# Kernel optimization log

Hardware: AMD Instinct MI355X
Metric: run time of the kernel (lower is better)

The kernel has to match this reference:

```python
import jax, jax.numpy as jnp
import numpy as np
import math

D_MODEL = 1024
N_HEADS = 16
QKV_DIM = 1024
D_HEAD = QKV_DIM // N_HEADS


def setup_inputs() -> dict:
    key = jax.random.key(0)
    ks = jax.random.split(key, 10)
    B, S = 4, 2048
    lim = 1.0 / math.sqrt(D_MODEL)
    lim_o = 1.0 / math.sqrt(QKV_DIM)
    return {
        "x": jax.random.normal(ks[0], (B, S, D_MODEL), dtype=jnp.float32),
        "w_q": jax.random.uniform(ks[1], (QKV_DIM, D_MODEL), minval=-lim, maxval=lim, dtype=jnp.float32),
        "b_q": jax.random.uniform(ks[2], (QKV_DIM,), minval=-lim, maxval=lim, dtype=jnp.float32),
        "w_k": jax.random.uniform(ks[3], (QKV_DIM, D_MODEL), minval=-lim, maxval=lim, dtype=jnp.float32),
        "b_k": jax.random.uniform(ks[4], (QKV_DIM,), minval=-lim, maxval=lim, dtype=jnp.float32),
        "w_v": jax.random.uniform(ks[5], (QKV_DIM, D_MODEL), minval=-lim, maxval=lim, dtype=jnp.float32),
        "b_v": jax.random.uniform(ks[6], (QKV_DIM,), minval=-lim, maxval=lim, dtype=jnp.float32),
        "w_o": jax.random.uniform(ks[7], (D_MODEL, QKV_DIM), minval=-lim_o, maxval=lim_o, dtype=jnp.float32),
        "b_o": jax.random.uniform(ks[8], (D_MODEL,), minval=-lim_o, maxval=lim_o, dtype=jnp.float32),
        "temperature": jnp.ones((1,), dtype=jnp.float32),
        "q_scale": jnp.ones((N_HEADS,), dtype=jnp.float32),
    }


def reference(x, w_q, b_q, w_k, b_k, w_v, b_v, w_o, b_o, temperature, q_scale):
    B, S, _ = x.shape
    # QKV projections: [B,S,qkv_dim] -> [B,H,S,Dh]
    def proj(w, b):
        y = jnp.einsum('bsd,ed->bse', x, w) + b
        return y.reshape(B, S, N_HEADS, D_HEAD).transpose(0, 2, 1, 3)
    q = proj(w_q, b_q)
    k = proj(w_k, b_k)
    v = proj(w_v, b_v)
    scale = jnp.sqrt(jnp.float32(D_HEAD)) * temperature[0]
    scores = jnp.einsum('bhqd,bhkd->bhqk', q, k) / scale
    attn = jax.nn.softmax(scores, axis=-1)
    attn = attn * q_scale.reshape(1, N_HEADS, 1, 1)  # per-head post-softmax scale
    out = jnp.einsum('bhqk,bhkd->bhqd', attn, v)
    out = out.transpose(0, 2, 1, 3).reshape(B, S, QKV_DIM)
    return jnp.einsum('bse,de->bsd', out, w_o) + b_o
```

## Files before the change

kernel.cpp:

```cpp
#include <hip/hip_runtime.h>
#include <hip/hip_bf16.h>
#include <stdint.h>

typedef __bf16 bf16;
typedef __bf16 bf16x8 __attribute__((ext_vector_type(8)));
typedef __bf16 bf16x4 __attribute__((ext_vector_type(4)));
typedef float f32x4 __attribute__((ext_vector_type(4)));
typedef float f32x16 __attribute__((ext_vector_type(16)));

#define NB 4
#define SEQ 2048
#define DM 1024
#define NHEADS 16
#define DHEAD 64
#define MTOK (NB*SEQ)
#define NE 3072

__device__ __forceinline__ void gl_lds16(const bf16* g, bf16* l) {
  __builtin_amdgcn_global_load_lds(
      (const __attribute__((address_space(1))) void*)g,
      (__attribute__((address_space(3))) void*)l, 16, 0, 0);
}

__device__ __forceinline__ f32x16 zero16() {
  f32x16 z;
#pragma unroll
  for (int i=0;i<16;i++) z[i]=0.f;
  return z;
}

__global__ __launch_bounds__(256) void convert_kernel(
    const float* __restrict__ x,
    const float* __restrict__ wq, const float* __restrict__ wk,
    const float* __restrict__ wv, const float* __restrict__ wo,
    const float* __restrict__ bq, const float* __restrict__ bk,
    const float* __restrict__ bv,
    bf16* __restrict__ xb, bf16* __restrict__ wqkvb,
    bf16* __restrict__ wob, float* __restrict__ bqkv) {
  int tid = blockIdx.x*blockDim.x + threadIdx.x;
  int nt = gridDim.x*blockDim.x;
  const int NX4 = MTOK*DM/4;
  for (int i = tid; i < NX4; i += nt) {
    float4 v = ((const float4*)x)[i];
    ((bf16x4*)xb)[i] = bf16x4{(bf16)v.x,(bf16)v.y,(bf16)v.z,(bf16)v.w};
  }
  const int NW4 = DM*DM/4;
  for (int i = tid; i < NW4; i += nt) {
    float4 a = ((const float4*)wq)[i];
    ((bf16x4*)wqkvb)[i] = bf16x4{(bf16)a.x,(bf16)a.y,(bf16)a.z,(bf16)a.w};
    float4 b = ((const float4*)wk)[i];
    ((bf16x4*)wqkvb)[i+NW4] = bf16x4{(bf16)b.x,(bf16)b.y,(bf16)b.z,(bf16)b.w};
    float4 c = ((const float4*)wv)[i];
    ((bf16x4*)wqkvb)[i+2*NW4] = bf16x4{(bf16)c.x,(bf16)c.y,(bf16)c.z,(bf16)c.w};
    float4 d = ((const float4*)wo)[i];
    ((bf16x4*)wob)[i] = bf16x4{(bf16)d.x,(bf16)d.y,(bf16)d.z,(bf16)d.w};
  }
  for (int i = tid; i < DM; i += nt) {
    bqkv[i] = bq[i]; bqkv[i+DM] = bk[i]; bqkv[i+2*DM] = bv[i];
  }
}

template<int OUT_MODE>
__global__ __launch_bounds__(256) void gemm_deep(
    const bf16* __restrict__ A, const bf16* __restrict__ Bm,
    const float* __restrict__ bias, void* __restrict__ Cout,
    int M, int N, int K) {
  __shared__ bf16 As[2][128*64];
  __shared__ bf16 Bs[2][128*64];
  const int bm = blockIdx.x, bn = blockIdx.y;
  const int thr = threadIdx.x;
  const int w = thr>>6, lane = thr&63;
  const int wr = w>>1, wc = w&1;
  const int l4 = lane>>4, lm = lane&15;
  f32x4 acc[4][4];
#pragma unroll
  for (int m=0;m<4;m++)
#pragma unroll
    for (int n=0;n<4;n++) acc[m][n] = f32x4{0.f,0.f,0.f,0.f};

  const bf16* Abase = A + (size_t)bm*128*K;
  const bf16* Bbase = Bm + (size_t)bn*128*K;

  const int srow = thr>>3;
  const int sch  = ((thr&7) ^ (srow&7)) * 8;
  const bf16* Ag = Abase + (size_t)srow*K + sch;
  const bf16* Bg = Bbase + (size_t)srow*K + sch;
  const int dbase = thr*8;

  const int nk = K>>6;

  int aoff[2][4], boff[2][4];
#pragma unroll
  for (int ks=0;ks<2;ks++) {
#pragma unroll
    for (int m=0;m<4;m++) {
      const int r = wr*64 + m*16 + lm;
      aoff[ks][m] = r*64 + ((((ks<<2)|l4) ^ (lm&7))*8);
    }
#pragma unroll
    for (int n=0;n<4;n++) {
      const int r = wc*64 + n*16 + lm;
      boff[ks][n] = r*64 + ((((ks<<2)|l4) ^ (lm&7))*8);
    }
  }

#pragma unroll
  for (int c=0;c<4;c++) {
    gl_lds16(Ag + (size_t)c*32*K, &As[0][c*2048 + dbase]);
    gl_lds16(Bg + (size_t)c*32*K, &Bs[0][c*2048 + dbase]);
  }

  for (int kt=0; kt<nk; ++kt) {
    const int p = kt&1;
    const int st = (kt+1 < nk) ? kt+1 : 0;
    const size_t ko = (size_t)st*64;
#pragma unroll
    for (int c=0;c<4;c++) {
      gl_lds16(Ag + ko + (size_t)c*32*K, &As[p^1][c*2048 + dbase]);
      gl_lds16(Bg + ko + (size_t)c*32*K, &Bs[p^1][c*2048 + dbase]);
    }
    asm volatile("s_waitcnt vmcnt(8)" ::: "memory");
    __builtin_amdgcn_s_barrier();
    __builtin_amdgcn_sched_barrier(0);

    const bf16* Ac = As[p];
    const bf16* Bc = Bs[p];
    __builtin_amdgcn_s_setprio(1);
#pragma unroll
    for (int ks=0;ks<2;ks++) {
      bf16x8 af[4], bfr[4];
#pragma unroll
      for (int m=0;m<4;m++) af[m] = *(const bf16x8*)&Ac[aoff[ks][m]];
#pragma unroll
      for (int n=0;n<4;n++) bfr[n] = *(const bf16x8*)&Bc[boff[ks][n]];
#pragma unroll
      for (int m=0;m<4;m++)
#pragma unroll
        for (int n=0;n<4;n++)
          acc[m][n] = __builtin_amdgcn_mfma_f32_16x16x32_bf16(af[m], bfr[n], acc[m][n], 0, 0, 0);
    }
    __builtin_amdgcn_s_setprio(0);
    __builtin_amdgcn_s_barrier();
    __builtin_amdgcn_sched_barrier(0);
  }

  const int rbase = bm*128 + wr*64 + l4*4;
  const int cbase = bn*128 + wc*64;
#pragma unroll
  for (int n=0;n<4;n++) {
    const int col = cbase + n*16 + lm;
    const float bv = bias[col];
#pragma unroll
    for (int m=0;m<4;m++) {
#pragma unroll
      for (int j=0;j<4;j++) {
        const int row = rbase + m*16 + j;
        const float v = acc[m][n][j] + bv;
        if (OUT_MODE == 0) ((bf16*)Cout)[(size_t)row*N + col] = (bf16)v;
        else               ((float*)Cout)[(size_t)row*N + col] = v;
      }
    }
  }
}

__global__ __launch_bounds__(256) void transpose_v(const bf16* __restrict__ qkv,
                                                   bf16* __restrict__ vt) {
  __shared__ bf16 tile[64*72];
  const int s0 = blockIdx.x*64;
  const int bh = blockIdx.y;
  const bf16* src = qkv + (size_t)((bh>>4)*SEQ + s0)*NE + 2*DM + (bh&15)*64;
  const int thr = threadIdx.x;
#pragma unroll
  for (int i=0;i<2;i++) {
    int idx = thr + i*256;
    int row = idx>>3, part = idx&7;
    *(bf16x8*)&tile[row*72 + part*8] = *(const bf16x8*)(src + (size_t)row*NE + part*8);
  }
  __syncthreads();
  bf16* dst = vt + (size_t)bh*64*SEQ + s0;
#pragma unroll
  for (int i=0;i<2;i++) {
    int idx = thr + i*256;
    int d = idx>>3, part = idx&7;
    bf16x8 v;
#pragma unroll
    for (int j=0;j<8;j++) v[j] = tile[(part*8+j)*72 + d];
    *(bf16x8*)(dst + (size_t)d*SEQ + part*8) = v;
  }
}

__global__ __launch_bounds__(256, 2) void attn_kernel(
    const bf16* __restrict__ qkv, const bf16* __restrict__ vt,
    bf16* __restrict__ aout,
    const float* __restrict__ temperature, const float* __restrict__ q_scale) {
  __shared__ bf16 smem[4][64*64];
  const int bh = blockIdx.y;
  const int b = bh>>4, h = bh&15;
  const int thr = threadIdx.x;
  const int w = thr>>6, lane = thr&63;
  const int l31 = lane&31, hi = lane>>5;
  const float sc2 = 1.4426950408889634f / (8.0f * temperature[0]);
  const int q0 = blockIdx.x*256 + w*64;
  const int NT = SEQ/64;
#define KBUFB 8192
#define VOFFB 16384

  bf16x8 qfA[4], qfB[4];
  {
    const bf16* qpA = qkv + (size_t)(b*SEQ + q0 + l31)*NE + h*64 + hi*8;
    const bf16* qpB = qpA + (size_t)32*NE;
#pragma unroll
    for (int s=0;s<4;s++) {
      bf16x8 qa = *(const bf16x8*)(qpA + s*16);
      bf16x8 qb = *(const bf16x8*)(qpB + s*16);
#pragma unroll
      for (int j=0;j<8;j++) {
        qfA[s][j] = (bf16)((float)qa[j] * sc2);
        qfB[s][j] = (bf16)((float)qb[j] * sc2);
      }
    }
  }

  f32x16 oA0 = zero16(), oA1 = zero16();
  f32x16 oB0 = zero16(), oB1 = zero16();
  float lpA = 0.f, lpB = 0.f;

  const bf16* Kbase = qkv + (size_t)b*SEQ*NE + DM + h*64;
  const bf16* Vbase = vt + (size_t)bh*64*SEQ;

  const int sr = thr>>2, scb = thr&3;
  const int wb0 = sr*128 + (((scb*2+0) ^ (sr&7))<<4);
  const int wb1 = sr*128 + (((scb*2+1) ^ (sr&7))<<4);
  const int rsw = l31&7;

  const char* kr0[4];
  const char* kr1[4];
#pragma unroll
  for (int s=0;s<4;s++) {
    const int slot = s*2 + hi;
    kr0[s] = (const char*)smem + l31*128      + ((slot ^ rsw)<<4);
    kr1[s] = (const char*)smem + (32+l31)*128 + ((slot ^ rsw)<<4);
  }

  const bf16* kgb = Kbase + (size_t)sr*NE + scb*16;
  const bf16* vgb = Vbase + (size_t)sr*SEQ + scb*16;

  bf16x8 ka, kb, va, vb;
  ka = *(const bf16x8*)(kgb);
  kb = *(const bf16x8*)(kgb + 8);
  va = *(const bf16x8*)(vgb);
  vb = *(const bf16x8*)(vgb + 8);
  *(bf16x8*)((char*)smem + wb0)         = ka;
  *(bf16x8*)((char*)smem + wb1)         = kb;
  *(bf16x8*)((char*)smem + VOFFB + wb0) = va;
  *(bf16x8*)((char*)smem + VOFFB + wb1) = vb;
  kgb += (size_t)64*NE; vgb += 64;
  ka = *(const bf16x8*)(kgb);
  kb = *(const bf16x8*)(kgb + 8);
  va = *(const bf16x8*)(vgb);
  vb = *(const bf16x8*)(vgb + 8);
  kgb += (size_t)64*NE; vgb += 64;
  __syncthreads();

#define MAKE_PU(PU, S0, S1, KS)                                                \
  { float e0,e1,e2,e3,e4,e5,e6,e7;                                             \
    if ((KS)==0)      { e0=S0[0]; e1=S0[1]; e2=S0[2]; e3=S0[3];                \
                        e4=S0[4]; e5=S0[5]; e6=S0[6]; e7=S0[7]; }              \
    else if ((KS)==1) { e0=S0[8]; e1=S0[9]; e2=S0[10];e3=S0[11];               \
                        e4=S0[12];e5=S0[13];e6=S0[14];e7=S0[15]; }             \
    else if ((KS)==2) { e0=S1[0]; e1=S1[1]; e2=S1[2]; e3=S1[3];                \
                        e4=S1[4]; e5=S1[5]; e6=S1[6]; e7=S1[7]; }              \
    else              { e0=S1[8]; e1=S1[9]; e2=S1[10];e3=S1[11];               \
                        e4=S1[12];e5=S1[13];e6=S1[14];e7=S1[15]; }             \
    unsigned a0,a1,b0,b1;                                                      \
    asm("v_cvt_pk_bf16_f32 %0, %1, %2" : "=v"(a0) : "v"(e0), "v"(e1));         \
    asm("v_cvt_pk_bf16_f32 %0, %1, %2" : "=v"(a1) : "v"(e2), "v"(e3));         \
    asm("v_cvt_pk_bf16_f32 %0, %1, %2" : "=v"(b0) : "v"(e4), "v"(e5));         \
    asm("v_cvt_pk_bf16_f32 %0, %1, %2" : "=v"(b1) : "v"(e6), "v"(e7));         \
    asm("v_permlane32_swap_b32 %0, %1" : "+v"(a0), "+v"(b0));                  \
    asm("v_permlane32_swap_b32 %0, %1" : "+v"(a1), "+v"(b1));                  \
    PU.u[0]=a0; PU.u[1]=a1; PU.u[2]=b0; PU.u[3]=b1; }

#define ATTN_TILE(P, T)                                                        \
  {                                                                            \
    const int t_ = (T);                                                        \
    if (t_ < NT-1) {                                                           \
      *(bf16x8*)((char*)smem + ((P)^1)*KBUFB + wb0)         = ka;              \
      *(bf16x8*)((char*)smem + ((P)^1)*KBUFB + wb1)         = kb;              \
      *(bf16x8*)((char*)smem + VOFFB + ((P)^1)*KBUFB + wb0) = va;              \
      *(bf16x8*)((char*)smem + VOFFB + ((P)^1)*KBUFB + wb1) = vb;              \
      if (t_ < NT-2) {                                                         \
        ka = *(const bf16x8*)(kgb);                                            \
        kb = *(const bf16x8*)(kgb + 8);                                        \
        va = *(const bf16x8*)(vgb);                                            \
        vb = *(const bf16x8*)(vgb + 8);                                        \
        kgb += (size_t)64*NE; vgb += 64;                                       \
      }                                                                        \
    }                                                                          \
    f32x16 sA0 = zero16(), sA1 = zero16(), sB0 = zero16(), sB1 = zero16();     \
    __builtin_amdgcn_s_setprio(1);                                             \
    _Pragma("unroll")                                                          \
    for (int s=0;s<4;s++) {                                                    \
      bf16x8 kf0 = *(const bf16x8*)(kr0[s] + (P)*KBUFB);                       \
      bf16x8 kf1 = *(const bf16x8*)(kr1[s] + (P)*KBUFB);                       \
      sA0 = __builtin_amdgcn_mfma_f32_32x32x16_bf16(kf0, qfA[s], sA0, 0,0,0);  \
      sB0 = __builtin_amdgcn_mfma_f32_32x32x16_bf16(kf0, qfB[s], sB0, 0,0,0);  \
      sA1 = __builtin_amdgcn_mfma_f32_32x32x16_bf16(kf1, qfA[s], sA1, 0,0,0);  \
      sB1 = __builtin_amdgcn_mfma_f32_32x32x16_bf16(kf1, qfB[s], sB1, 0,0,0);  \
    }                                                                          \
    __builtin_amdgcn_s_setprio(0);                                             \
    _Pragma("unroll")                                                          \
    for (int r=0;r<16;r++) { sA0[r] = __builtin_amdgcn_exp2f(sA0[r]); lpA += sA0[r]; } \
    _Pragma("unroll")                                                          \
    for (int r=0;r<16;r++) { sA1[r] = __builtin_amdgcn_exp2f(sA1[r]); lpA += sA1[r]; } \
    _Pragma("unroll")                                                          \
    for (int r=0;r<16;r++) { sB0[r] = __builtin_amdgcn_exp2f(sB0[r]); lpB += sB0[r]; } \
    _Pragma("unroll")                                                          \
    for (int r=0;r<16;r++) { sB1[r] = __builtin_amdgcn_exp2f(sB1[r]); lpB += sB1[r]; } \
    __builtin_amdgcn_s_setprio(1);                                             \
    _Pragma("unroll")                                                          \
    for (int ks=0;ks<4;ks++) {                                                 \
      union { unsigned u[4]; bf16x8 v; } puA, puB;                             \
      MAKE_PU(puA, sA0, sA1, ks);                                              \
      MAKE_PU(puB, sB0, sB1, ks);                                              \
      bf16x8 vf0, vf1;                                                         \
      if (ks==0) { vf0 = *(const bf16x8*)(kr0[0] + VOFFB + (P)*KBUFB);         \
                   vf1 = *(const bf16x8*)(kr1[0] + VOFFB + (P)*KBUFB); }       \
      else if (ks==1) { vf0 = *(const bf16x8*)(kr0[1] + VOFFB + (P)*KBUFB);    \
                   vf1 = *(const bf16x8*)(kr1[1] + VOFFB + (P)*KBUFB); }       \
      else if (ks==2) { vf0 = *(const bf16x8*)(kr0[2] + VOFFB + (P)*KBUFB);    \
                   vf1 = *(const bf16x8*)(kr1[2] + VOFFB + (P)*KBUFB); }       \
      else { vf0 = *(const bf16x8*)(kr0[3] + VOFFB + (P)*KBUFB);               \
             vf1 = *(const bf16x8*)(kr1[3] + VOFFB + (P)*KBUFB); }             \
      oA0 = __builtin_amdgcn_mfma_f32_32x32x16_bf16(puA.v, vf0, oA0, 0,0,0);   \
      oA1 = __builtin_amdgcn_mfma_f32_32x32x16_bf16(puA.v, vf1, oA1, 0,0,0);   \
      oB0 = __builtin_amdgcn_mfma_f32_32x32x16_bf16(puB.v, vf0, oB0, 0,0,0);   \
      oB1 = __builtin_amdgcn_mfma_f32_32x32x16_bf16(puB.v, vf1, oB1, 0,0,0);   \
    }                                                                          \
    __builtin_amdgcn_s_setprio(0);                                             \
    __syncthreads();                                                           \
  }

  for (int t2=0; t2<NT/2; ++t2) {
    ATTN_TILE(0, 2*t2);
    ATTN_TILE(1, 2*t2+1);
  }
#undef ATTN_TILE
#undef MAKE_PU

  lpA += __shfl_xor(lpA, 32);
  lpB += __shfl_xor(lpB, 32);
  const float qs = q_scale[h];
  const float ivA_lane = qs / lpA;
  const float ivB_lane = qs / lpB;
#pragma unroll
  for (int r=0;r<16;r++) {
    const int qi = (r&3) + 8*(r>>2) + hi*4;
    {
      const float iv = __shfl(ivA_lane, qi);
      bf16* op = aout + (size_t)(b*SEQ + q0 + qi)*DM + h*64 + l31;
      op[0]  = (bf16)(oA0[r]*iv);
      op[32] = (bf16)(oA1[r]*iv);
    }
    {
      const float iv = __shfl(ivB_lane, qi);
      bf16* op = aout + (size_t)(b*SEQ + q0 + 32 + qi)*DM + h*64 + l31;
      op[0]  = (bf16)(oB0[r]*iv);
      op[32] = (bf16)(oB1[r]*iv);
    }
  }
}

extern "C" void kernel_launch(void* const* d_in, const int* in_sizes, int n_in,
                              void* d_out, int out_size, void* d_ws, size_t ws_size,
                              hipStream_t stream) {
  (void)in_sizes; (void)n_in; (void)out_size; (void)ws_size;
  const float* x  = (const float*)d_in[0];
  const float* wq = (const float*)d_in[1];
  const float* bq = (const float*)d_in[2];
  const float* wk = (const float*)d_in[3];
  const float* bk = (const float*)d_in[4];
  const float* wv = (const float*)d_in[5];
  const float* bv = (const float*)d_in[6];
  const float* wo = (const float*)d_in[7];
  const float* bo = (const float*)d_in[8];
  const float* temp = (const float*)d_in[9];
  const float* qsc  = (const float*)d_in[10];

  char* ws = (char*)d_ws;
  bf16* xb    = (bf16*)ws; ws += (size_t)MTOK*DM*2;
  bf16* wqkvb = (bf16*)ws; ws += (size_t)NE*DM*2;
  bf16* wob   = (bf16*)ws; ws += (size_t)DM*DM*2;
  float* bqkv = (float*)ws; ws += (size_t)NE*4;
  bf16* qkv   = (bf16*)ws; ws += (size_t)MTOK*NE*2;
  bf16* vt    = (bf16*)ws; ws += (size_t)NB*NHEADS*DHEAD*SEQ*2;
  bf16* aout  = (bf16*)ws; ws += (size_t)MTOK*DM*2;

  convert_kernel<<<dim3(1024), dim3(256), 0, stream>>>(x, wq, wk, wv, wo, bq, bk, bv,
                                                       xb, wqkvb, wob, bqkv);
  gemm_deep<0><<<dim3(MTOK/128, NE/128), dim3(256), 0, stream>>>(xb, wqkvb, bqkv, qkv,
                                                                 MTOK, NE, DM);
  transpose_v<<<dim3(SEQ/64, NB*NHEADS), dim3(256), 0, stream>>>(qkv, vt);
  attn_kernel<<<dim3(SEQ/256, NB*NHEADS), dim3(256), 0, stream>>>(qkv, vt, aout, temp, qsc);
  gemm_deep<1><<<dim3(MTOK/128, DM/128), dim3(256), 0, stream>>>(aout, wob, bo, d_out,
                                                                 MTOK, DM, DM);
}
```

Baseline: 179.9 us.

## Split attention over two KV halves and add a combine kernel

Measured after the change: 640.4 us. +256.0%, slower.

```diff
diff --git a/kernel.cpp b/kernel.cpp
--- a/kernel.cpp
+++ b/kernel.cpp
@@ -189,19 +189,20 @@
   }
 }
 
-__global__ __launch_bounds__(256, 2) void attn_kernel(
+__global__ __launch_bounds__(256, 4) void attn_kernel(
     const bf16* __restrict__ qkv, const bf16* __restrict__ vt,
-    bf16* __restrict__ aout,
-    const float* __restrict__ temperature, const float* __restrict__ q_scale) {
+    bf16* __restrict__ po, float* __restrict__ lp,
+    const float* __restrict__ temperature) {
   __shared__ bf16 smem[4][64*64];
   const int bh = blockIdx.y;
+  const int kvh = blockIdx.z;
   const int b = bh>>4, h = bh&15;
   const int thr = threadIdx.x;
   const int w = thr>>6, lane = thr&63;
   const int l31 = lane&31, hi = lane>>5;
   const float sc2 = 1.4426950408889634f / (8.0f * temperature[0]);
   const int q0 = blockIdx.x*256 + w*64;
-  const int NT = SEQ/64;
+  const int NT = SEQ/64/2;
 #define KBUFB 8192
 #define VOFFB 16384
 
@@ -225,8 +226,8 @@
   f32x16 oB0 = zero16(), oB1 = zero16();
   float lpA = 0.f, lpB = 0.f;
 
-  const bf16* Kbase = qkv + (size_t)b*SEQ*NE + DM + h*64;
-  const bf16* Vbase = vt + (size_t)bh*64*SEQ;
+  const bf16* Kbase = qkv + (size_t)b*SEQ*NE + DM + h*64 + (size_t)(kvh*1024)*NE;
+  const bf16* Vbase = vt + (size_t)bh*64*SEQ + kvh*1024;
 
   const int sr = thr>>2, scb = thr&3;
   const int wb0 = sr*128 + (((scb*2+0) ^ (sr&7))<<4);
@@ -350,25 +351,43 @@
 
   lpA += __shfl_xor(lpA, 32);
   lpB += __shfl_xor(lpB, 32);
-  const float qs = q_scale[h];
-  const float ivA_lane = qs / lpA;
-  const float ivB_lane = qs / lpB;
+  bf16* pob = po + (size_t)kvh*MTOK*DM;
 #pragma unroll
   for (int r=0;r<16;r++) {
     const int qi = (r&3) + 8*(r>>2) + hi*4;
     {
-      const float iv = __shfl(ivA_lane, qi);
-      bf16* op = aout + (size_t)(b*SEQ + q0 + qi)*DM + h*64 + l31;
-      op[0]  = (bf16)(oA0[r]*iv);
-      op[32] = (bf16)(oA1[r]*iv);
+      bf16* op = pob + (size_t)(b*SEQ + q0 + qi)*DM + h*64 + l31;
+      op[0]  = (bf16)oA0[r];
+      op[32] = (bf16)oA1[r];
     }
     {
-      const float iv = __shfl(ivB_lane, qi);
-      bf16* op = aout + (size_t)(b*SEQ + q0 + 32 + qi)*DM + h*64 + l31;
-      op[0]  = (bf16)(oB0[r]*iv);
-      op[32] = (bf16)(oB1[r]*iv);
-    }
-  }
+      bf16* op = pob + (size_t)(b*SEQ + q0 + 32 + qi)*DM + h*64 + l31;
+      op[0]  = (bf16)oB0[r];
+      op[32] = (bf16)oB1[r];
+    }
+  }
+  if (hi == 0) {
+    lp[((size_t)kvh*MTOK + b*SEQ + q0 + l31)*NHEADS + h]      = lpA;
+    lp[((size_t)kvh*MTOK + b*SEQ + q0 + 32 + l31)*NHEADS + h] = lpB;
+  }
+}
+
+__global__ __launch_bounds__(256) void combine_kernel(
+    const bf16* __restrict__ po, const float* __restrict__ lp,
+    const float* __restrict__ q_scale, bf16* __restrict__ aout) {
+  const int idx = blockIdx.x*256 + threadIdx.x;
+  const int token = idx >> 7;
+  const int d8 = idx & 127;
+  const int d0 = d8 * 8;
+  const int h = d8 >> 3;
+  bf16x8 a = *(const bf16x8*)(po + (size_t)token*DM + d0);
+  bf16x8 b = *(const bf16x8*)(po + (size_t)MTOK*DM + (size_t)token*DM + d0);
+  const float l = lp[(size_t)token*NHEADS + h] + lp[((size_t)MTOK + token)*NHEADS + h];
+  const float iv = q_scale[h] / l;
+  bf16x8 o;
+#pragma unroll
+  for (int j=0;j<8;j++) o[j] = (bf16)(((float)a[j] + (float)b[j]) * iv);
+  *(bf16x8*)(aout + (size_t)token*DM + d0) = o;
 }
 
 extern "C" void kernel_launch(void* const* d_in, const int* in_sizes, int n_in,
@@ -395,13 +414,16 @@
   bf16* qkv   = (bf16*)ws; ws += (size_t)MTOK*NE*2;
   bf16* vt    = (bf16*)ws; ws += (size_t)NB*NHEADS*DHEAD*SEQ*2;
   bf16* aout  = (bf16*)ws; ws += (size_t)MTOK*DM*2;
+  bf16* po    = (bf16*)ws; ws += (size_t)2*MTOK*DM*2;
+  float* lp   = (float*)ws; ws += (size_t)2*MTOK*NHEADS*4;
 
   convert_kernel<<<dim3(1024), dim3(256), 0, stream>>>(x, wq, wk, wv, wo, bq, bk, bv,
                                                        xb, wqkvb, wob, bqkv);
   gemm_deep<0><<<dim3(MTOK/128, NE/128), dim3(256), 0, stream>>>(xb, wqkvb, bqkv, qkv,
                                                                  MTOK, NE, DM);
   transpose_v<<<dim3(SEQ/64, NB*NHEADS), dim3(256), 0, stream>>>(qkv, vt);
-  attn_kernel<<<dim3(SEQ/256, NB*NHEADS), dim3(256), 0, stream>>>(qkv, vt, aout, temp, qsc);
+  attn_kernel<<<dim3(SEQ/256, NB*NHEADS, 2), dim3(256), 0, stream>>>(qkv, vt, po, lp, temp);
+  combine_kernel<<<dim3(MTOK*DM/8/256), dim3(256), 0, stream>>>(po, lp, qsc, aout);
   gemm_deep<1><<<dim3(MTOK/128, DM/128), dim3(256), 0, stream>>>(aout, wob, bo, d_out,
                                                                  MTOK, DM, DM);
 }
```
